# Kernel optimization log

Hardware: AMD Instinct MI355X
Metric: run time of the kernel (lower is better)

## Reference

```python
import jax, jax.numpy as jnp
import numpy as np

B, C, H, W = 8, 16, 1024, 1024
ALPHA = 0.2  # contamination weight per neighbor


def setup_inputs() -> dict:
    key = jax.random.key(0)
    x = jax.random.normal(key, (B, C, H, W), dtype=jnp.float32)
    return {"x": x}


def reference(x):
    # Original module: for every grid cell (src), add 0.2*x[src] to each of its
    # 8 in-bounds neighbors in y (y initialized to x, x never mutated).
    # Scatter-to-neighbors == gather-from-neighbors: y = x + 0.2 * sum of 8 neighbors.
    xp = jnp.pad(x, ((0, 0), (0, 0), (1, 1), (1, 1)))  # zero pad -> out-of-bounds skipped
    nb = (
        xp[:, :, 0:-2, 1:-1] + xp[:, :, 2:, 1:-1] +      # up, down
        xp[:, :, 1:-1, 0:-2] + xp[:, :, 1:-1, 2:] +      # left, right
        xp[:, :, 0:-2, 0:-2] + xp[:, :, 0:-2, 2:] +      # diagonals
        xp[:, :, 2:, 0:-2] + xp[:, :, 2:, 2:]
    )
    return x + ALPHA * nb
```

## Files before the change

kernel.cpp:

```cpp
#include <hip/hip_runtime.h>
#include <hip/hip_bf16.h>


#define ALPHA 0.2f
#define ROWS 16

typedef float f4 __attribute__((ext_vector_type(4)));

__device__ __forceinline__ void load6(const float* __restrict__ p, int w, int W,
                                      float v[6]) {
    const f4 c = *reinterpret_cast<const f4*>(p + w);
    v[0] = (w > 0) ? p[w - 1] : 0.0f;
    v[1] = c.x; v[2] = c.y; v[3] = c.z; v[4] = c.w;
    v[5] = (w + 4 < W) ? p[w + 4] : 0.0f;
}

__global__ __launch_bounds__(256)
void contamination_kernel(const float* __restrict__ x, float* __restrict__ y,
                          int H, int W) {
    const int tilesPerImg = H / ROWS;
    const int tile = blockIdx.x;
    const int img  = tile / tilesPerImg;
    const int h0   = (tile - img * tilesPerImg) * ROWS;
    const size_t base = ((size_t)img * H + (size_t)h0) * W;
    const int w = threadIdx.x * 4;

    const float* __restrict__ row = x + base;
    float* __restrict__ orow = y + base;

    float t[6], m[6], b[6];
#pragma unroll
    for (int j = 0; j < 6; ++j) t[j] = 0.0f;

    if (h0 > 0) load6(row - W, w, W, t);
    load6(row, w, W, m);

#pragma unroll
    for (int i = 0; i < ROWS; ++i) {
        if (h0 + i + 1 < H) {
            load6(row + W, w, W, b);
        } else {
#pragma unroll
            for (int j = 0; j < 6; ++j) b[j] = 0.0f;
        }

        f4 o;
#pragma unroll
        for (int j = 0; j < 4; ++j) {
            const float nb = t[j] + t[j + 1] + t[j + 2] +
                             b[j] + b[j + 1] + b[j + 2] +
                             m[j] + m[j + 2];
            o[j] = m[j + 1] + ALPHA * nb;
        }
        __builtin_nontemporal_store(o, reinterpret_cast<f4*>(orow + w));

#pragma unroll
        for (int j = 0; j < 6; ++j) { t[j] = m[j]; m[j] = b[j]; }
        row += W; orow += W;
    }
}

extern "C" void kernel_launch(void* const* d_in, const int* in_sizes, int n_in,
                              void* d_out, int out_size, void* d_ws, size_t ws_size,
                              hipStream_t stream) {
    const float* x = (const float*)d_in[0];
    float* y = (float*)d_out;

    const int W = 1024;
    const int H = 1024;
    const int n = in_sizes[0];
    const int blocks = n / (W * ROWS);

    contamination_kernel<<<dim3(blocks), dim3(W / 4), 0, stream>>>(x, y, H, W);
}
```

Measured before the change: 203.7 us.

## Deepen row tiles, prefetch two rows ahead, reuse horizontal 3-sums

Each block now covers 32 rows instead of 16, which halves the number of redundant halo rows loaded per image. Loads are issued two rows ahead so more memory requests are in flight while the current row is computed. Each row's horizontal 3-tap sum is computed once and reused across the three output rows that need it, and W and H become compile-time constants. The kernel launches half as many blocks and each thread holds more registers, which can lower occupancy and parallelism.

```diff
diff --git a/kernel.cpp b/kernel.cpp
--- a/kernel.cpp
+++ b/kernel.cpp
@@ -3,11 +3,13 @@
 
 
 #define ALPHA 0.2f
-#define ROWS 16
+#define ROWS 32
+#define W 1024
+#define H 1024
 
 typedef float f4 __attribute__((ext_vector_type(4)));
 
-__device__ __forceinline__ void load6(const float* __restrict__ p, int w, int W,
+__device__ __forceinline__ void load6(const float* __restrict__ p, int w,
                                       float v[6]) {
     const f4 c = *reinterpret_cast<const f4*>(p + w);
     v[0] = (w > 0) ? p[w - 1] : 0.0f;
@@ -15,47 +17,64 @@
     v[5] = (w + 4 < W) ? p[w + 4] : 0.0f;
 }
 
+__device__ __forceinline__ void sums(const float v[6], f4& s, f4& c) {
+    const float p12 = v[1] + v[2], p34 = v[3] + v[4];
+    s.x = v[0] + p12;  s.y = p12 + v[3];
+    s.z = v[2] + p34;  s.w = p34 + v[5];
+    c.x = v[1]; c.y = v[2]; c.z = v[3]; c.w = v[4];
+}
+
 __global__ __launch_bounds__(256)
-void contamination_kernel(const float* __restrict__ x, float* __restrict__ y,
-                          int H, int W) {
+void contamination_kernel(const float* __restrict__ x, float* __restrict__ y) {
     const int tilesPerImg = H / ROWS;
     const int tile = blockIdx.x;
     const int img  = tile / tilesPerImg;
     const int h0   = (tile - img * tilesPerImg) * ROWS;
-    const size_t base = ((size_t)img * H + (size_t)h0) * W;
+    const size_t base = ((size_t)img * H + (size_t)h0) * (size_t)W;
     const int w = threadIdx.x * 4;
 
-    const float* __restrict__ row = x + base;
-    float* __restrict__ orow = y + base;
+    const float* __restrict__ row  = x + base;
+    float* __restrict__       orow = y + base;
 
-    float t[6], m[6], b[6];
-#pragma unroll
-    for (int j = 0; j < 6; ++j) t[j] = 0.0f;
+    f4 t_s, m_s, m_c;
+    {
+        float v[6];
+        if (h0 > 0) {
+            load6(row - W, w, v);
+            f4 dc; sums(v, t_s, dc);
+        } else {
+            t_s.x = t_s.y = t_s.z = t_s.w = 0.0f;
+        }
+        load6(row, w, v);
+        sums(v, m_s, m_c);
+    }
 
-    if (h0 > 0) load6(row - W, w, W, t);
-    load6(row, w, W, m);
+    float p1[6], p2[6];
+    load6(row + W, w, p1);
+    load6(row + 2 * W, w, p2);
 
 #pragma unroll
     for (int i = 0; i < ROWS; ++i) {
-        if (h0 + i + 1 < H) {
-            load6(row + W, w, W, b);
+        f4 b_s, b_c;
+        sums(p1, b_s, b_c);
+
+#pragma unroll
+        for (int j = 0; j < 6; ++j) p1[j] = p2[j];
+
+        if (i < ROWS - 2 && h0 + i + 3 < H) {
+            load6(row + 3 * W, w, p2);
         } else {
 #pragma unroll
-            for (int j = 0; j < 6; ++j) b[j] = 0.0f;
+            for (int j = 0; j < 6; ++j) p2[j] = 0.0f;
         }
 
         f4 o;
 #pragma unroll
-        for (int j = 0; j < 4; ++j) {
-            const float nb = t[j] + t[j + 1] + t[j + 2] +
-                             b[j] + b[j + 1] + b[j + 2] +
-                             m[j] + m[j + 2];
-            o[j] = m[j + 1] + ALPHA * nb;
-        }
+        for (int j = 0; j < 4; ++j)
+            o[j] = fmaf(ALPHA, t_s[j] + m_s[j] + b_s[j] - m_c[j], m_c[j]);
         __builtin_nontemporal_store(o, reinterpret_cast<f4*>(orow + w));
 
-#pragma unroll
-        for (int j = 0; j < 6; ++j) { t[j] = m[j]; m[j] = b[j]; }
+        t_s = m_s; m_s = b_s; m_c = b_c;
         row += W; orow += W;
     }
 }
@@ -66,10 +85,8 @@
     const float* x = (const float*)d_in[0];
     float* y = (float*)d_out;
 
-    const int W = 1024;
-    const int H = 1024;
     const int n = in_sizes[0];
-    const int blocks = n / (W * ROWS);
+    const int blocks = (n / W) / ROWS;
 
-    contamination_kernel<<<dim3(blocks), dim3(W / 4), 0, stream>>>(x, y, H, W);
+    contamination_kernel<<<dim3(blocks), dim3(W / 4), 0, stream>>>(x, y);
 }
```

Result: slower. 213.7 us (+4.9%).
